# Kernel optimization log

Measured on AMD Instinct MI355X. Metric: run time of the kernel, lower is better.

The kernel has to match this reference:

```python
import jax, jax.numpy as jnp
import numpy as np

EPS = 1e-5
NH = 8          # num_heads
WT_LEVELS = 5


def ln(x, w, b):
    m = jnp.mean(x, -1, keepdims=True)
    v = jnp.mean((x - m) ** 2, -1, keepdims=True)
    return (x - m) / jnp.sqrt(v + EPS) * w + b


def gelu(x):
    return jax.nn.gelu(x, approximate=False)  # torch nn.GELU default (erf)


def dwconv(x, w, b, stride, padding):
    # x: [B,C,H,W], w: [kh,kw,1,C] depthwise
    C = x.shape[1]
    y = jax.lax.conv_general_dilated(x, w, (stride, stride), padding,
                                     dimension_numbers=('NCHW', 'HWIO', 'NCHW'),
                                     feature_group_count=C)
    return y if b is None else y + b[None, :, None, None]


def conv2d(x, w, b, padding='SAME'):
    y = jax.lax.conv_general_dilated(x, w, (1, 1), padding,
                                     dimension_numbers=('NCHW', 'HWIO', 'NCHW'))
    return y + b[None, :, None, None]


def haar_dwt(x):
    # orthonormal 2x2 Haar analysis via even/odd slicing (no conv needed)
    a = x[..., 0::2, 0::2]; b = x[..., 0::2, 1::2]
    c = x[..., 1::2, 0::2]; d = x[..., 1::2, 1::2]
    ll = (a + b + c + d) * 0.5
    lh = (-a - b + c + d) * 0.5
    hl = (-a + b - c + d) * 0.5
    hh = (a - b - c + d) * 0.5
    return ll, lh, hl, hh


def haar_idwt(ll, lh, hl, hh):
    a = (ll - lh - hl + hh) * 0.5
    b = (ll - lh + hl - hh) * 0.5
    c = (ll + lh - hl - hh) * 0.5
    d = (ll + lh + hl + hh) * 0.5
    B, C, H, W = ll.shape
    top = jnp.stack([a, b], -1).reshape(B, C, H, 2 * W)
    bot = jnp.stack([c, d], -1).reshape(B, C, H, 2 * W)
    return jnp.stack([top, bot], -2).reshape(B, C, 2 * H, 2 * W)


def wtconv(x, base_w, base_b, base_scale, wav_w, wav_scale):
    # WTConv2d (Haar, wt_levels=5, kernel 3, depthwise): multi-level wavelet
    # decomposition, depthwise 3x3 conv + scale at each level, reconstruction,
    # added to a scaled depthwise base conv.
    B, C = x.shape[0], x.shape[1]
    lls, hs, shapes = [], [], []
    cur = x
    for i in range(WT_LEVELS):
        shapes.append(cur.shape)
        Hc, Wc = cur.shape[2], cur.shape[3]
        if Hc % 2 or Wc % 2:
            cur = jnp.pad(cur, ((0, 0), (0, 0), (0, Hc % 2), (0, Wc % 2)))
        sub = jnp.stack(haar_dwt(cur), 2)                # [B,C,4,h,w]
        cur = sub[:, :, 0]
        h, w = sub.shape[3], sub.shape[4]
        t = sub.reshape(B, C * 4, h, w)
        t = dwconv(t, wav_w[i], None, 1, 'SAME') * wav_scale[i][None, :, None, None]
        t = t.reshape(B, C, 4, h, w)
        lls.append(t[:, :, 0])
        hs.append(t[:, :, 1:4])
    nxt = 0.0
    for i in range(WT_LEVELS - 1, -1, -1):
        ll = lls[i] + nxt
        h3 = hs[i]
        nxt = haar_idwt(ll, h3[:, :, 0], h3[:, :, 1], h3[:, :, 2])
        sh = shapes[i]
        nxt = nxt[:, :, :sh[2], :sh[3]]
    base = dwconv(x, base_w, base_b, 1, 'SAME') * base_scale[None, :, None, None]
    return base + nxt


def block_forward(x, H, W, ln1_w, ln1_b, ln2_w, ln2_b, q_w, kv1_w, kv2_w,
                  sr1_w, sr1_b, sr2_w, sr2_b, an1_w, an1_b, an2_w, an2_b,
                  wt_base_w, wt_base_b, wt_base_scale, wt_wav_w, wt_wav_scale,
                  cp2d_w, cp2d_b, cn_w, cn_b, proj_w, proj_b,
                  fc1_w, fc1_b, fc2_w, fc2_b):
    B, N, C0 = x.shape
    Cp = C0 // 4            # conv/wavelet part channels
    Ca = C0 - Cp            # attention part channels (3/4)
    hd = Ca // NH
    scale = hd ** -0.5

    xin = ln(x, ln1_w, ln1_b)
    xc, xa = xin[..., :Cp], xin[..., Cp:]

    # --- wavelet-conv branch ---
    xc = xc.reshape(B, H, W, Cp).transpose(0, 3, 1, 2)        # [B,Cp,H,W]
    xc = wtconv(xc, wt_base_w, wt_base_b, wt_base_scale, wt_wav_w, wt_wav_scale)
    xc = conv2d(xc, cp2d_w, cp2d_b, 'SAME')                   # k3 p1 (sr_ratio=8)
    xc = gelu(ln(xc.reshape(B, Cp, N).transpose(0, 2, 1), cn_w, cn_b))  # [B,N,Cp]

    # --- multi-scale spatial-reduction attention (sr_ratio=8) ---
    q = (xa @ q_w).reshape(B, N, NH, hd).transpose(0, 2, 1, 3)  # [B,NH,N,hd]
    x_ = xa.transpose(0, 2, 1).reshape(B, Ca, H, W)
    x1 = gelu(ln(dwconv(x_, sr1_w, sr1_b, 8, 'VALID').reshape(B, Ca, -1)
                 .transpose(0, 2, 1), an1_w, an1_b))           # [B,49,Ca]
    x2 = gelu(ln(dwconv(x_, sr2_w, sr2_b, 4, 'VALID').reshape(B, Ca, -1)
                 .transpose(0, 2, 1), an2_w, an2_b))           # [B,196,Ca]

    def branch(xs, kv_w, qh):
        L = xs.shape[1]
        kv = (xs @ kv_w).reshape(B, L, 2, NH // 2, hd).transpose(2, 0, 3, 1, 4)
        k, v = kv[0], kv[1]
        a = jax.nn.softmax(jnp.einsum('bhnd,bhld->bhnl', qh, k) * scale, axis=-1)
        return jnp.einsum('bhnl,bhld->bhnd', a, v).transpose(0, 2, 1, 3).reshape(B, N, Ca // 2)

    y1 = branch(x1, kv1_w, q[:, :NH // 2])
    y2 = branch(x2, kv2_w, q[:, NH // 2:])

    attn_out = jnp.concatenate([y1, y2, xc], -1) @ proj_w + proj_b

    x = x + attn_out
    m = ln(x, ln2_w, ln2_b)
    return x + (gelu(m @ fc1_w + fc1_b) @ fc2_w + fc2_b)


def setup_inputs() -> dict:
    key = jax.random.key(0)
    ks = jax.random.split(key, 16)
    B, H, W, C0 = 32, 56, 56, 128
    N = H * W
    Cp, Ca = C0 // 4, C0 // 4 * 3

    def nrm(k, shape, std=0.02):
        return jax.random.normal(k, shape, jnp.float32) * std

    return dict(
        x=jax.random.normal(ks[0], (B, N, C0), jnp.float32),
        H=H, W=W,
        ln1_w=jnp.ones((C0,)), ln1_b=jnp.zeros((C0,)),
        ln2_w=jnp.ones((C0,)), ln2_b=jnp.zeros((C0,)),
        q_w=nrm(ks[1], (Ca, Ca)),
        kv1_w=nrm(ks[2], (Ca, Ca)),
        kv2_w=nrm(ks[3], (Ca, Ca)),
        sr1_w=nrm(ks[4], (8, 8, 1, Ca), 0.05), sr1_b=jnp.zeros((Ca,)),
        sr2_w=nrm(ks[5], (4, 4, 1, Ca), 0.05), sr2_b=jnp.zeros((Ca,)),
        an1_w=jnp.ones((Ca,)), an1_b=jnp.zeros((Ca,)),
        an2_w=jnp.ones((Ca,)), an2_b=jnp.zeros((Ca,)),
        wt_base_w=nrm(ks[6], (3, 3, 1, Cp), 0.1), wt_base_b=jnp.zeros((Cp,)),
        wt_base_scale=jnp.ones((Cp,)),
        wt_wav_w=nrm(ks[7], (5, 3, 3, 1, 4 * Cp), 0.1),
        wt_wav_scale=jnp.full((5, 4 * Cp), 0.1, jnp.float32),
        cp2d_w=nrm(ks[8], (3, 3, Cp, Cp), 0.05), cp2d_b=jnp.zeros((Cp,)),
        cn_w=jnp.ones((Cp,)), cn_b=jnp.zeros((Cp,)),
        proj_w=nrm(ks[9], (C0, C0)), proj_b=jnp.zeros((C0,)),
        fc1_w=nrm(ks[10], (C0, 4 * C0)), fc1_b=jnp.zeros((4 * C0,)),
        fc2_w=nrm(ks[11], (4 * C0, C0)), fc2_b=jnp.zeros((C0,)),
    )


def reference(x, H, W, ln1_w, ln1_b, ln2_w, ln2_b, q_w, kv1_w, kv2_w,
              sr1_w, sr1_b, sr2_w, sr2_b, an1_w, an1_b, an2_w, an2_b,
              wt_base_w, wt_base_b, wt_base_scale, wt_wav_w, wt_wav_scale,
              cp2d_w, cp2d_b, cn_w, cn_b, proj_w, proj_b,
              fc1_w, fc1_b, fc2_w, fc2_b):
    return block_forward(x, H, W, ln1_w, ln1_b, ln2_w, ln2_b, q_w, kv1_w, kv2_w,
                         sr1_w, sr1_b, sr2_w, sr2_b, an1_w, an1_b, an2_w, an2_b,
                         wt_base_w, wt_base_b, wt_base_scale, wt_wav_w, wt_wav_scale,
                         cp2d_w, cp2d_b, cn_w, cn_b, proj_w, proj_b,
                         fc1_w, fc1_b, fc2_w, fc2_b)
```

## Files before the change

### kernel.cpp

```cpp
#include <hip/hip_runtime.h>
#include <hip/hip_bf16.h>
#include <math.h>

typedef __hip_bfloat16 bf16;
typedef __attribute__((ext_vector_type(8))) short bf16x8;
typedef __attribute__((ext_vector_type(4))) float f32x4;

#define Bc   32
#define Hc   56
#define Wcc  56
#define Nc   3136
#define Cpc  32
#define Cac  96
#define EPSc 1e-5f
#define SCALEc 0.28867513459481287f

__device__ __forceinline__ float gelu_f(float x) {
    return 0.5f * x * (1.0f + erff(x * 0.7071067811865475f));
}

__device__ __forceinline__ float fast_exp2(float x) {
#if defined(__has_builtin)
#if __has_builtin(__builtin_amdgcn_exp2f)
    return __builtin_amdgcn_exp2f(x);
#else
    return exp2f(x);
#endif
#else
    return exp2f(x);
#endif
}

__global__ __launch_bounds__(256) void ln1_kernel(const float* __restrict__ x,
        const float* __restrict__ g, const float* __restrict__ be,
        float* __restrict__ xa, bf16* __restrict__ xab, float* __restrict__ xc_img)
{
    int wv = threadIdx.x >> 6, lane = threadIdx.x & 63;
    int row = blockIdx.x * 4 + wv;
    if (row >= Bc * Nc) return;
    const float* xr = x + (size_t)row * 128;
    float x0 = xr[lane];
    float x1 = xr[lane + 64];
    float s = x0 + x1, q = x0 * x0 + x1 * x1;
    for (int o = 32; o; o >>= 1) { s += __shfl_xor(s, o); q += __shfl_xor(q, o); }
    float mean = s * (1.f / 128.f);
    float inv = rsqrtf(q * (1.f / 128.f) - mean * mean + EPSc);
    int b = row / Nc, n = row % Nc;
    {
        int c = lane;
        float y = (x0 - mean) * inv * g[c] + be[c];
        if (c < Cpc) xc_img[(size_t)(b * Cpc + c) * Nc + n] = y;
        else { xa[(size_t)row * Cac + (c - Cpc)] = y;
               xab[(size_t)row * Cac + (c - Cpc)] = __float2bfloat16(y); }
    }
    {
        int c = lane + 64;
        float y = (x1 - mean) * inv * g[c] + be[c];
        xa[(size_t)row * Cac + (c - Cpc)] = y;
        xab[(size_t)row * Cac + (c - Cpc)] = __float2bfloat16(y);
    }
}

__global__ void dwt_kernel(const float* __restrict__ src, int cs, int h, int w,
                           int h2, int w2, float* __restrict__ sub)
{
    int t = blockIdx.x * blockDim.x + threadIdx.x;
    int total = Bc * 32 * h2 * w2;
    if (t >= total) return;
    int xx = t % w2; int r = t / w2;
    int yy = r % h2; r /= h2;
    int c = r & 31; int b = r >> 5;
    const float* sp = src + (size_t)cs * (b * 32 + c) * h * w;
    int y0 = yy * 2, x0 = xx * 2;
    bool xe = (x0 + 1 < w), ye = (y0 + 1 < h);
    float a  = sp[y0 * w + x0];
    float bb = xe ? sp[y0 * w + x0 + 1] : 0.f;
    float cc = ye ? sp[(y0 + 1) * w + x0] : 0.f;
    float dd = (xe && ye) ? sp[(y0 + 1) * w + x0 + 1] : 0.f;
    size_t pl = (size_t)h2 * w2;
    size_t ob = (size_t)(b * 128 + c * 4) * pl + yy * w2 + xx;
    sub[ob]          = ( a + bb + cc + dd) * 0.5f;
    sub[ob + pl]     = (-a - bb + cc + dd) * 0.5f;
    sub[ob + 2 * pl] = (-a + bb - cc + dd) * 0.5f;
    sub[ob + 3 * pl] = ( a - bb - cc + dd) * 0.5f;
}

__global__ __launch_bounds__(256) void dwt234_kernel(const float* __restrict__ S1,
        float* __restrict__ S2, float* __restrict__ S3, float* __restrict__ S4)
{
    __shared__ float ll[196];
    int bc = blockIdx.x; int b = bc >> 5, c = bc & 31;
    int t = threadIdx.x;
    const float* src = S1 + (size_t)(b * 128 + c * 4) * 196;
    if (t < 196) ll[t] = src[t];
    __syncthreads();
    float l2 = 0.f;
    if (t < 49) {
        int yy = t / 7, xx = t % 7;
        int y0 = yy * 2, x0 = xx * 2;
        float a = ll[y0 * 14 + x0],       bb = ll[y0 * 14 + x0 + 1];
        float cc = ll[(y0 + 1) * 14 + x0], dd = ll[(y0 + 1) * 14 + x0 + 1];
        size_t ob = (size_t)(b * 128 + c * 4) * 49 + t;
        float vll = (a + bb + cc + dd) * 0.5f;
        S2[ob]       = vll;
        S2[ob + 49]  = (-a - bb + cc + dd) * 0.5f;
        S2[ob + 98]  = (-a + bb - cc + dd) * 0.5f;
        S2[ob + 147] = ( a - bb - cc + dd) * 0.5f;
        l2 = vll;
    }
    __syncthreads();
    if (t < 49) ll[t] = l2;
    __syncthreads();
    float l3 = 0.f;
    if (t < 16) {
        int yy = t >> 2, xx = t & 3;
        int y0 = yy * 2, x0 = xx * 2;
        bool xe = (x0 + 1 < 7), ye = (y0 + 1 < 7);
        float a  = ll[y0 * 7 + x0];
        float bb = xe ? ll[y0 * 7 + x0 + 1] : 0.f;
        float cc = ye ? ll[(y0 + 1) * 7 + x0] : 0.f;
        float dd = (xe && ye) ? ll[(y0 + 1) * 7 + x0 + 1] : 0.f;
        size_t ob = (size_t)(b * 128 + c * 4) * 16 + t;
        float vll = (a + bb + cc + dd) * 0.5f;
        S3[ob]      = vll;
        S3[ob + 16] = (-a - bb + cc + dd) * 0.5f;
        S3[ob + 32] = (-a + bb - cc + dd) * 0.5f;
        S3[ob + 48] = ( a - bb - cc + dd) * 0.5f;
        l3 = vll;
    }
    __syncthreads();
    if (t < 16) ll[t] = l3;
    __syncthreads();
    if (t < 4) {
        int yy = t >> 1, xx = t & 1;
        int y0 = yy * 2, x0 = xx * 2;
        float a = ll[y0 * 4 + x0],       bb = ll[y0 * 4 + x0 + 1];
        float cc = ll[(y0 + 1) * 4 + x0], dd = ll[(y0 + 1) * 4 + x0 + 1];
        size_t ob = (size_t)(b * 128 + c * 4) * 4 + t;
        S4[ob]      = ( a + bb + cc + dd) * 0.5f;
        S4[ob + 4]  = (-a - bb + cc + dd) * 0.5f;
        S4[ob + 8]  = (-a + bb - cc + dd) * 0.5f;
        S4[ob + 12] = ( a - bb - cc + dd) * 0.5f;
    }
}

template<int H>
__device__ __forceinline__ void dw3_body(int r, const float* __restrict__ src,
        const float* __restrict__ wt, const float* __restrict__ scale,
        float* __restrict__ dst)
{
    int x = r % H; int rr = r / H;
    int y = rr % H; rr /= H;
    int c = rr & 127;
    const float* sp = src + (r - x - y * H);
    float acc = 0.f;
    #pragma unroll
    for (int u = 0; u < 3; u++) {
        int yy = y + u - 1;
        if (yy < 0 || yy >= H) continue;
        #pragma unroll
        for (int v = 0; v < 3; v++) {
            int xx = x + v - 1;
            if (xx < 0 || xx >= H) continue;
            acc += sp[yy * H + xx] * wt[(u * 3 + v) * 128 + c];
        }
    }
    dst[r] = acc * scale[c];
}

__global__ void dw3x3_all_kernel(const float* __restrict__ sub, const float* __restrict__ wavw,
        const float* __restrict__ wavs, float* __restrict__ tt)
{
    int t = blockIdx.x * blockDim.x + threadIdx.x;
    if (t < 3211264)      dw3_body<28>(t,           sub,           wavw,        wavs,       tt);
    else if (t < 4014080) dw3_body<14>(t - 3211264, sub + 3211264, wavw + 1152, wavs + 128, tt + 3211264);
    else if (t < 4214784) dw3_body<7> (t - 4014080, sub + 4014080, wavw + 2304, wavs + 256, tt + 4014080);
    else if (t < 4280320) dw3_body<4> (t - 4214784, sub + 4214784, wavw + 3456, wavs + 384, tt + 4214784);
    else if (t < 4296704) dw3_body<2> (t - 4280320, sub + 4280320, wavw + 4608, wavs + 512, tt + 4280320);
}

__global__ __launch_bounds__(256) void idwt432_kernel(const float* __restrict__ T4,
        const float* __restrict__ T3, const float* __restrict__ T2,
        float* __restrict__ out14)
{
    __shared__ float rec[196];
    int bc = blockIdx.x; int b = bc >> 5, c = bc & 31;
    int t = threadIdx.x;
    float v4 = 0.f;
    if (t < 16) {
        int y = t >> 2, x = t & 3;
        int y2 = y >> 1, x2 = x >> 1;
        size_t base = (size_t)(b * 128 + c * 4) * 4 + y2 * 2 + x2;
        float ll = T4[base];
        float lh = T4[base + 4], hl = T4[base + 8], hh = T4[base + 12];
        float v;
        if ((y & 1) == 0) v = ((x & 1) == 0) ? (ll - lh - hl + hh) : (ll - lh + hl - hh);
        else              v = ((x & 1) == 0) ? (ll + lh - hl - hh) : (ll + lh + hl + hh);
        v4 = v * 0.5f;
    }
    if (t < 16) rec[t] = v4;
    __syncthreads();
    float v3 = 0.f;
    if (t < 49) {
        int y = t / 7, x = t % 7;
        int y2 = y >> 1, x2 = x >> 1;
        size_t base = (size_t)(b * 128 + c * 4) * 16 + y2 * 4 + x2;
        float ll = T3[base] + rec[y2 * 4 + x2];
        float lh = T3[base + 16], hl = T3[base + 32], hh = T3[base + 48];
        float v;
        if ((y & 1) == 0) v = ((x & 1) == 0) ? (ll - lh - hl + hh) : (ll - lh + hl - hh);
        else              v = ((x & 1) == 0) ? (ll + lh - hl - hh) : (ll + lh + hl + hh);
        v3 = v * 0.5f;
    }
    __syncthreads();
    if (t < 49) rec[t] = v3;
    __syncthreads();
    if (t < 196) {
        int y = t / 14, x = t % 14;
        int y2 = y >> 1, x2 = x >> 1;
        size_t base = (size_t)(b * 128 + c * 4) * 49 + y2 * 7 + x2;
        float ll = T2[base] + rec[y2 * 7 + x2];
        float lh = T2[base + 49], hl = T2[base + 98], hh = T2[base + 147];
        float v;
        if ((y & 1) == 0) v = ((x & 1) == 0) ? (ll - lh - hl + hh) : (ll - lh + hl - hh);
        else              v = ((x & 1) == 0) ? (ll + lh - hl - hh) : (ll + lh + hl + hh);
        out14[(size_t)(b * 32 + c) * 196 + t] = v * 0.5f;
    }
}

__global__ void idwt_kernel(const float* __restrict__ tl, const float* __restrict__ nxt,
        float* __restrict__ outp, int h2, int w2, int ho, int wo)
{
    int t = blockIdx.x * blockDim.x + threadIdx.x;
    int total = Bc * 32 * ho * wo;
    if (t >= total) return;
    int x = t % wo; int r = t / wo;
    int y = r % ho; r /= ho;
    int c = r & 31; int b = r >> 5;
    int y2 = y >> 1, x2 = x >> 1;
    size_t pl = (size_t)h2 * w2;
    size_t base = (size_t)(b * 128 + c * 4) * pl + y2 * w2 + x2;
    float ll = tl[base];
    if (nxt) ll += nxt[(size_t)(b * 32 + c) * pl + y2 * w2 + x2];
    float lh = tl[base + pl], hl = tl[base + 2 * pl], hh = tl[base + 3 * pl];
    float v;
    if ((y & 1) == 0) v = ((x & 1) == 0) ? (ll - lh - hl + hh) : (ll - lh + hl - hh);
    else              v = ((x & 1) == 0) ? (ll + lh - hl - hh) : (ll + lh + hl + hh);
    outp[t] = v * 0.5f;
}

__global__ void idwt_dwbase_kernel(const float* __restrict__ tl, const float* __restrict__ nxt,
        const float* __restrict__ src, const float* __restrict__ wt,
        const float* __restrict__ scale, const float* __restrict__ bias,
        bf16* __restrict__ dst_nhwc)
{
    int t = blockIdx.x * blockDim.x + threadIdx.x;
    if (t >= Bc * 32 * Nc) return;
    int x = t % Wcc; int r = t / Wcc;
    int y = r % Hc; r /= Hc;
    int c = r & 31; int b = r >> 5;
    int y2 = y >> 1, x2 = x >> 1;
    const size_t pl = 784;
    size_t base = (size_t)(b * 128 + c * 4) * pl + y2 * 28 + x2;
    float ll = tl[base] + nxt[(size_t)(b * 32 + c) * pl + y2 * 28 + x2];
    float lh = tl[base + pl], hl = tl[base + 2 * pl], hh = tl[base + 3 * pl];
    float v;
    if ((y & 1) == 0) v = ((x & 1) == 0) ? (ll - lh - hl + hh) : (ll - lh + hl - hh);
    else              v = ((x & 1) == 0) ? (ll + lh - hl - hh) : (ll + lh + hl + hh);
    float recon = v * 0.5f;
    const float* sp = src + (t - x - y * Wcc);
    float acc = 0.f;
    #pragma unroll
    for (int u = 0; u < 3; u++) {
        int yy = y + u - 1;
        if (yy < 0 || yy >= Hc) continue;
        #pragma unroll
        for (int vv2 = 0; vv2 < 3; vv2++) {
            int xx = x + vv2 - 1;
            if (xx < 0 || xx >= Wcc) continue;
            acc += sp[yy * Wcc + xx] * wt[(u * 3 + vv2) * 32 + c];
        }
    }
    acc = (acc + bias[c]) * scale[c] + recon;
    dst_nhwc[(((size_t)b * Hc + y) * Wcc + x) * 32 + c] = __float2bfloat16(acc);
}

__global__ void wprep_kernel(const float* __restrict__ qw, const float* __restrict__ kv1w,
        const float* __restrict__ kv2w, const float* __restrict__ pw,
        const float* __restrict__ f1w, const float* __restrict__ f2w,
        const float* __restrict__ cpw, bf16* __restrict__ qwt, bf16* __restrict__ kv1wt,
        bf16* __restrict__ kv2wt, bf16* __restrict__ pwt, bf16* __restrict__ w1t,
        bf16* __restrict__ w2t, bf16* __restrict__ cpwt)
{
    int t = blockIdx.x * blockDim.x + threadIdx.x;
    if (t < 9216) {
        int n = t % 96, k = t / 96;
        qwt[n * 96 + k] = __float2bfloat16(qw[t]);
    } else if (t < 18432) {
        int u = t - 9216; int n = u % 96, k = u / 96;
        kv1wt[n * 96 + k] = __float2bfloat16(kv1w[u]);
    } else if (t < 27648) {
        int u = t - 18432; int n = u % 96, k = u / 96;
        kv2wt[n * 96 + k] = __float2bfloat16(kv2w[u]);
    } else if (t < 44032) {
        int u = t - 27648; int n = u % 128, k = u / 128;
        pwt[n * 128 + k] = __float2bfloat16(pw[u]);
    } else if (t < 109568) {
        int u = t - 44032; int n = u % 512, k = u / 512;
        w1t[(size_t)n * 128 + k] = __float2bfloat16(f1w[u]);
    } else if (t < 175104) {
        int u = t - 109568; int n = u % 128, k = u / 128;
        w2t[(size_t)n * 512 + k] = __float2bfloat16(f2w[u]);
    } else if (t < 184320) {
        int u = t - 175104; int co = u / 288, k = u % 288;
        cpwt[u] = __float2bfloat16(cpw[k * 32 + co]);
    }
}

__global__ __launch_bounds__(256) void cp2d_cn_kernel(const bf16* __restrict__ src,
        const bf16* __restrict__ wtc, const float* __restrict__ bias,
        const float* __restrict__ cnw, const float* __restrict__ cnb,
        bf16* __restrict__ attn_cat)
{
    __shared__ unsigned short in_s[10 * 400];
    __shared__ unsigned short w_s[32 * 296];
    int tid = threadIdx.x;
    int b = blockIdx.y;
    int ty = blockIdx.x / 7, tx = blockIdx.x % 7;
    for (int idx = tid; idx < 1152; idx += 256) {
        int co = idx / 36, j8 = (idx % 36) * 8;
        *(int4*)&w_s[co * 296 + j8] = *(const int4*)(wtc + co * 288 + j8);
    }
    {
        int idx = tid;
        if (idx < 200) {
            int cell = idx >> 1, half = idx & 1;
            int dy = cell / 10, dx = cell % 10;
            int gy = ty * 8 - 1 + dy, gx = tx * 8 - 1 + dx;
            int4 v0 = make_int4(0, 0, 0, 0), v1 = v0;
            if (gy >= 0 && gy < 56 && gx >= 0 && gx < 56) {
                const int4* gp = (const int4*)(src + ((((size_t)b * 56 + gy) * 56 + gx) * 32 + half * 16));
                v0 = gp[0]; v1 = gp[1];
            }
            *(int4*)&in_s[dy * 400 + dx * 40 + half * 16] = v0;
            *(int4*)&in_s[dy * 400 + dx * 40 + half * 16 + 8] = v1;
        }
    }
    __syncthreads();
    int wave = tid >> 6, lane = tid & 63;
    int ml = lane & 15, qd = lane >> 4;
    int m = wave * 16 + ml;
    int ly = m >> 3, lx = m & 7;
    f32x4 acc0 = {0.f, 0.f, 0.f, 0.f}, acc1 = {0.f, 0.f, 0.f, 0.f};
    #pragma unroll
    for (int u = 0; u < 3; u++)
    #pragma unroll
    for (int v = 0; v < 3; v++) {
        bf16x8 af = *(const bf16x8*)&in_s[(ly + u) * 400 + (lx + v) * 40 + qd * 8];
        int k = (u * 3 + v) * 32 + qd * 8;
        bf16x8 b0 = *(const bf16x8*)&w_s[ml * 296 + k];
        bf16x8 b1 = *(const bf16x8*)&w_s[(16 + ml) * 296 + k];
        acc0 = __builtin_amdgcn_mfma_f32_16x16x32_bf16(af, b0, acc0, 0, 0, 0);
        acc1 = __builtin_amdgcn_mfma_f32_16x16x32_bf16(af, b1, acc1, 0, 0, 0);
    }
    float bia0 = bias[ml], bia1 = bias[16 + ml];
    float g0 = cnw[ml], g1 = cnw[16 + ml];
    float be0 = cnb[ml], be1 = cnb[16 + ml];
    #pragma unroll
    for (int r = 0; r < 4; r++) {
        float c0 = acc0[r] + bia0;
        float c1 = acc1[r] + bia1;
        float s = c0 + c1, q = c0 * c0 + c1 * c1;
        #pragma unroll
        for (int o = 8; o; o >>= 1) { s += __shfl_xor(s, o); q += __shfl_xor(q, o); }
        float mean = s * (1.f / 32.f);
        float inv = rsqrtf(q * (1.f / 32.f) - mean * mean + EPSc);
        int mr = wave * 16 + qd * 4 + r;
        int ry = ty * 8 + (mr >> 3), rx = tx * 8 + (mr & 7);
        bf16* op = attn_cat + ((size_t)b * Nc + ry * 56 + rx) * 128 + 96;
        op[ml]      = __float2bfloat16(gelu_f((c0 - mean) * inv * g0 + be0));
        op[16 + ml] = __float2bfloat16(gelu_f((c1 - mean) * inv * g1 + be1));
    }
}

template<int KS, int LD>
__device__ __forceinline__ void sr_body(int t, const float* __restrict__ xa,
        const float* __restrict__ wt, const float* __restrict__ bias,
        float* __restrict__ outp)
{
    int c = t % Cac; int r = t / Cac;
    int j = r % LD; r /= LD;
    int i = r % LD; int b = r / LD;
    float acc = bias[c];
    for (int u = 0; u < KS; u++)
        for (int v = 0; v < KS; v++)
            acc += xa[(size_t)(b * Nc + (i * KS + u) * Wcc + (j * KS + v)) * Cac + c]
                 * wt[(u * KS + v) * Cac + c];
    outp[t] = acc;
}

__global__ void sr_all_kernel(const float* __restrict__ xa,
        const float* __restrict__ sr1w, const float* __restrict__ sr1b, float* __restrict__ x1p,
        const float* __restrict__ sr2w, const float* __restrict__ sr2b, float* __restrict__ x2p)
{
    int t = blockIdx.x * blockDim.x + threadIdx.x;
    if (t < 150528) sr_body<8, 7>(t, xa, sr1w, sr1b, x1p);
    else {
        int u = t - 150528;
        if (u < 602112) sr_body<4, 14>(u, xa, sr2w, sr2b, x2p);
    }
}

__global__ __launch_bounds__(256) void ln96_all_kernel(
        const float* __restrict__ s1, const float* __restrict__ g1,
        const float* __restrict__ b1, bf16* __restrict__ d1,
        const float* __restrict__ s2, const float* __restrict__ g2,
        const float* __restrict__ b2, bf16* __restrict__ d2)
{
    int wv = threadIdx.x >> 6, lane = threadIdx.x & 63;
    int row = blockIdx.x * 4 + wv;
    const float* sp; const float* g; const float* be; bf16* dst; int r;
    if (row < 1568)      { sp = s1; g = g1; be = b1; dst = d1; r = row; }
    else if (row < 7840) { sp = s2; g = g2; be = b2; dst = d2; r = row - 1568; }
    else return;
    sp += (size_t)r * 96;
    float x0 = sp[lane];
    float x1 = (lane < 32) ? sp[64 + lane] : 0.f;
    float s = x0 + x1, q = x0 * x0 + x1 * x1;
    for (int o = 32; o; o >>= 1) { s += __shfl_xor(s, o); q += __shfl_xor(q, o); }
    float mean = s * (1.f / 96.f);
    float inv = rsqrtf(q * (1.f / 96.f) - mean * mean + EPSc);
    dst[(size_t)r * 96 + lane] =
        __float2bfloat16(gelu_f((x0 - mean) * inv * g[lane] + be[lane]));
    if (lane < 32)
        dst[(size_t)r * 96 + 64 + lane] =
            __float2bfloat16(gelu_f((x1 - mean) * inv * g[64 + lane] + be[64 + lane]));
}

template<int OMODE>
__device__ __forceinline__ void qkv_body(const bf16* __restrict__ A,
        const bf16* __restrict__ Wt, void* __restrict__ outp,
        int M, int m0, unsigned short (*As)[40], unsigned short (*Bs)[40], int tid)
{
    const int K = 96, Nt = 96;
    int wave = tid >> 6, lane = tid & 63;
    f32x4 acc[6];
    #pragma unroll
    for (int f = 0; f < 6; f++) acc[f] = (f32x4){0.f, 0.f, 0.f, 0.f};
    int ar = tid >> 2, ac = (tid & 3) << 3;
    int ml = wave * 16 + (lane & 15);
    int qd = lane >> 4;
    for (int k0 = 0; k0 < K; k0 += 32) {
        int4 av = make_int4(0, 0, 0, 0);
        if (m0 + ar < M) av = *(const int4*)(A + (size_t)(m0 + ar) * K + k0 + ac);
        *(int4*)&As[ar][ac] = av;
        for (int idx = tid; idx < 384; idx += 256) {
            int br = idx >> 2, bc = (idx & 3) << 3;
            *(int4*)&Bs[br][bc] = *(const int4*)(Wt + (size_t)br * K + k0 + bc);
        }
        __syncthreads();
        bf16x8 af = *(const bf16x8*)&As[ml][qd * 8];
        #pragma unroll
        for (int f = 0; f < 6; f++) {
            bf16x8 bfv = *(const bf16x8*)&Bs[f * 16 + (lane & 15)][qd * 8];
            acc[f] = __builtin_amdgcn_mfma_f32_16x16x32_bf16(af, bfv, acc[f], 0, 0, 0);
        }
        __syncthreads();
    }
    #pragma unroll
    for (int f = 0; f < 6; f++) {
        int n = f * 16 + (lane & 15);
        #pragma unroll
        for (int r = 0; r < 4; r++) {
            int m = m0 + wave * 16 + qd * 4 + r;
            if (m >= M) continue;
            float v = acc[f][r];
            if (OMODE == 2) {
                int b = m / Nc, nn = m - b * Nc;
                int h = n / 12, d = n - h * 12;
                ((float*)outp)[(((size_t)(b * 8 + h)) * Nc + nn) * 12 + d] = v;
            } else
                ((float*)outp)[(size_t)m * Nt + n] = v;
        }
    }
}

__global__ __launch_bounds__(256) void qkv_kernel(
        const bf16* __restrict__ XAb,  const bf16* __restrict__ qwt,   float* __restrict__ QB,
        const bf16* __restrict__ X1Bb, const bf16* __restrict__ kv1wt, float* __restrict__ KV1,
        const bf16* __restrict__ X2Bb, const bf16* __restrict__ kv2wt, float* __restrict__ KV2)
{
    __shared__ unsigned short As[64][40];
    __shared__ unsigned short Bs[96][40];
    int by = blockIdx.x;
    int tid = threadIdx.x;
    if (by < 1568)      qkv_body<2>(XAb,  qwt,   QB,  100352, by * 64,          As, Bs, tid);
    else if (by < 1593) qkv_body<0>(X1Bb, kv1wt, KV1, 1568,   (by - 1568) * 64, As, Bs, tid);
    else                qkv_body<0>(X2Bb, kv2wt, KV2, 6272,   (by - 1593) * 64, As, Bs, tid);
}

template<int NF, int BK, bool GELU, bool RES, int OMODE>
__global__ __launch_bounds__(256) void gemm_kernel(const bf16* __restrict__ A,
        const bf16* __restrict__ Wt, const float* __restrict__ bias,
        const float* __restrict__ res, void* __restrict__ outp,
        int M, int K, int Nt)
{
    constexpr int TN = 16 * NF;
    __shared__ unsigned short As[64][BK + 8];
    __shared__ unsigned short Bs[TN][BK + 8];
    int tid = threadIdx.x;
    int wave = tid >> 6, lane = tid & 63;
    int m0 = blockIdx.y * 64, n0 = blockIdx.x * TN;
    f32x4 acc[NF];
    #pragma unroll
    for (int f = 0; f < NF; f++) acc[f] = (f32x4){0.f, 0.f, 0.f, 0.f};

    int ar = tid >> 2, ac = (tid & 3) << 3;
    int ml = wave * 16 + (lane & 15);
    int qd = lane >> 4;

    for (int k0 = 0; k0 < K; k0 += BK) {
        #pragma unroll
        for (int i = 0; i < BK / 32; i++) {
            int cc = ac + i * 32;
            int4 av = make_int4(0, 0, 0, 0);
            if (m0 + ar < M) av = *(const int4*)(A + (size_t)(m0 + ar) * K + k0 + cc);
            *(int4*)&As[ar][cc] = av;
        }
        for (int idx = tid; idx < TN * (BK / 8); idx += 256) {
            int br = idx / (BK / 8), bc = (idx % (BK / 8)) * 8;
            *(int4*)&Bs[br][bc] = *(const int4*)(Wt + (size_t)(n0 + br) * K + k0 + bc);
        }
        __syncthreads();
        #pragma unroll
        for (int kk = 0; kk < BK / 32; kk++) {
            bf16x8 af = *(const bf16x8*)&As[ml][kk * 32 + qd * 8];
            #pragma unroll
            for (int f = 0; f < NF; f++) {
                bf16x8 bfv = *(const bf16x8*)&Bs[f * 16 + (lane & 15)][kk * 32 + qd * 8];
                acc[f] = __builtin_amdgcn_mfma_f32_16x16x32_bf16(af, bfv, acc[f], 0, 0, 0);
            }
        }
        __syncthreads();
    }
    #pragma unroll
    for (int f = 0; f < NF; f++) {
        int n = n0 + f * 16 + (lane & 15);
        #pragma unroll
        for (int r = 0; r < 4; r++) {
            int m = m0 + wave * 16 + qd * 4 + r;
            if (m >= M) continue;
            float v = acc[f][r];
            if (bias) v += bias[n];
            if (GELU) v = gelu_f(v);
            if (RES)  v += res[(size_t)m * Nt + n];
            if (OMODE == 1)
                ((bf16*)outp)[(size_t)m * Nt + n] = __float2bfloat16(v);
            else
                ((float*)outp)[(size_t)m * Nt + n] = v;
        }
    }
}

__global__ __launch_bounds__(256) void proj_ln_kernel(const bf16* __restrict__ A,
        const bf16* __restrict__ Wt, const float* __restrict__ bias,
        const float* __restrict__ res, const float* __restrict__ g,
        const float* __restrict__ be, float* __restrict__ xres, bf16* __restrict__ xnb)
{
    __shared__ unsigned short As[64][72];
    __shared__ unsigned short Bs[128][72];
    int tid = threadIdx.x;
    int wave = tid >> 6, lane = tid & 63;
    int m0 = blockIdx.x * 64;
    f32x4 acc[8];
    #pragma unroll
    for (int f = 0; f < 8; f++) acc[f] = (f32x4){0.f, 0.f, 0.f, 0.f};

    int ar = tid >> 2, ac = (tid & 3) << 3;
    int ml = lane & 15, qd = lane >> 4;
    int mlw = wave * 16 + ml;

    for (int k0 = 0; k0 < 128; k0 += 64) {
        #pragma unroll
        for (int i = 0; i < 2; i++) {
            int cc = ac + i * 32;
            *(int4*)&As[ar][cc] = *(const int4*)(A + (size_t)(m0 + ar) * 128 + k0 + cc);
        }
        for (int idx = tid; idx < 1024; idx += 256) {
            int br = idx >> 3, bc = (idx & 7) * 8;
            *(int4*)&Bs[br][bc] = *(const int4*)(Wt + (size_t)br * 128 + k0 + bc);
        }
        __syncthreads();
        #pragma unroll
        for (int kk = 0; kk < 2; kk++) {
            bf16x8 af = *(const bf16x8*)&As[mlw][kk * 32 + qd * 8];
            #pragma unroll
            for (int f = 0; f < 8; f++) {
                bf16x8 bfv = *(const bf16x8*)&Bs[f * 16 + ml][kk * 32 + qd * 8];
                acc[f] = __builtin_amdgcn_mfma_f32_16x16x32_bf16(af, bfv, acc[f], 0, 0, 0);
            }
        }
        __syncthreads();
    }
    float bia[8], gg[8], bb[8];
    #pragma unroll
    for (int f = 0; f < 8; f++) {
        int n = f * 16 + ml;
        bia[f] = bias[n]; gg[f] = g[n]; bb[f] = be[n];
    }
    #pragma unroll
    for (int r = 0; r < 4; r++) {
        int m = m0 + wave * 16 + qd * 4 + r;
        float vv[8];
        float s = 0.f, q = 0.f;
        #pragma unroll
        for (int f = 0; f < 8; f++) {
            int n = f * 16 + ml;
            float v = acc[f][r] + bia[f] + res[(size_t)m * 128 + n];
            vv[f] = v; s += v; q += v * v;
        }
        #pragma unroll
        for (int o = 8; o; o >>= 1) { s += __shfl_xor(s, o); q += __shfl_xor(q, o); }
        float mean = s * (1.f / 128.f);
        float inv = rsqrtf(q * (1.f / 128.f) - mean * mean + EPSc);
        #pragma unroll
        for (int f = 0; f < 8; f++) {
            int n = f * 16 + ml;
            xres[(size_t)m * 128 + n] = vv[f];
            xnb[(size_t)m * 128 + n] =
                __float2bfloat16((vv[f] - mean) * inv * gg[f] + bb[f]);
        }
    }
}

template<int L>
__device__ __forceinline__ void attn_body(const float* __restrict__ qh,
        const float* __restrict__ kv, int hl, int h, int b,
        float* kb, float* vb, bf16* __restrict__ attn_cat)
{
    for (int idx = threadIdx.x; idx < L * 3; idx += 256) {
        int l = idx / 3, f = idx % 3;
        const float4* kp = (const float4*)(kv + (size_t)(b * L + l) * 96 + hl * 12) + f;
        float4 kk = kp[0];
        float4 vv = kp[12];
        *(float4*)&kb[l * 12 + f * 4] = kk;
        *(float4*)&vb[l * 12 + f * 4] = vv;
    }
    int n = blockIdx.x * 256 + threadIdx.x;
    bool act = (n < Nc);
    int nn = act ? n : (Nc - 1);
    const float4* qp = (const float4*)(qh + (((size_t)(b * 8 + h)) * Nc + nn) * 12);
    float4 q0 = qp[0], q1 = qp[1], q2 = qp[2];
    const float PRE = SCALEc * 1.4426950408889634f;
    q0.x *= PRE; q0.y *= PRE; q0.z *= PRE; q0.w *= PRE;
    q1.x *= PRE; q1.y *= PRE; q1.z *= PRE; q1.w *= PRE;
    q2.x *= PRE; q2.y *= PRE; q2.z *= PRE; q2.w *= PRE;
    __syncthreads();

    float den = 0.f;
    float o[12];
    #pragma unroll
    for (int d = 0; d < 12; d++) o[d] = 0.f;

    #pragma unroll 4
    for (int l = 0; l < L; l++) {
        const float4 k0 = *(const float4*)&kb[l * 12];
        const float4 k1 = *(const float4*)&kb[l * 12 + 4];
        const float4 k2 = *(const float4*)&kb[l * 12 + 8];
        float s0 = q0.x * k0.x + q0.y * k0.y + q0.z * k0.z + q0.w * k0.w;
        float s1 = q1.x * k1.x + q1.y * k1.y + q1.z * k1.z + q1.w * k1.w;
        float s2 = q2.x * k2.x + q2.y * k2.y + q2.z * k2.z + q2.w * k2.w;
        float e = fast_exp2(s0 + s1 + s2);
        den += e;
        const float4 v0 = *(const float4*)&vb[l * 12];
        const float4 v1 = *(const float4*)&vb[l * 12 + 4];
        const float4 v2 = *(const float4*)&vb[l * 12 + 8];
        o[0] += e * v0.x; o[1]  += e * v0.y; o[2]  += e * v0.z; o[3]  += e * v0.w;
        o[4] += e * v1.x; o[5]  += e * v1.y; o[6]  += e * v1.z; o[7]  += e * v1.w;
        o[8] += e * v2.x; o[9]  += e * v2.y; o[10] += e * v2.z; o[11] += e * v2.w;
    }
    if (act) {
        float rden = 1.f / den;
        bf16* op = attn_cat + (size_t)(b * Nc + n) * 128 + h * 12;
        #pragma unroll
        for (int d = 0; d < 12; d++) op[d] = __float2bfloat16(o[d] * rden);
    }
}

__global__ __launch_bounds__(256) void attn_kernel(const float* __restrict__ qh,
        const float* __restrict__ kv1, const float* __restrict__ kv2,
        bf16* __restrict__ attn_cat)
{
    __shared__ float kb[196 * 12];
    __shared__ float vb[196 * 12];
    int h = blockIdx.y, b = blockIdx.z;
    if (h < 4) attn_body<49> (qh, kv1, h,     h, b, kb, vb, attn_cat);
    else       attn_body<196>(qh, kv2, h - 4, h, b, kb, vb, attn_cat);
}

extern "C" void kernel_launch(void* const* d_in, const int* in_sizes, int n_in,
                              void* d_out, int out_size, void* d_ws, size_t ws_size,
                              hipStream_t stream)
{
    const float* x    = (const float*)d_in[0];
    const float* ln1w = (const float*)d_in[3];
    const float* ln1b = (const float*)d_in[4];
    const float* ln2w = (const float*)d_in[5];
    const float* ln2b = (const float*)d_in[6];
    const float* qw   = (const float*)d_in[7];
    const float* kv1w = (const float*)d_in[8];
    const float* kv2w = (const float*)d_in[9];
    const float* sr1w = (const float*)d_in[10];
    const float* sr1b = (const float*)d_in[11];
    const float* sr2w = (const float*)d_in[12];
    const float* sr2b = (const float*)d_in[13];
    const float* an1w = (const float*)d_in[14];
    const float* an1b = (const float*)d_in[15];
    const float* an2w = (const float*)d_in[16];
    const float* an2b = (const float*)d_in[17];
    const float* wbw  = (const float*)d_in[18];
    const float* wbb  = (const float*)d_in[19];
    const float* wbs  = (const float*)d_in[20];
    const float* wavw = (const float*)d_in[21];
    const float* wavs = (const float*)d_in[22];
    const float* cpw  = (const float*)d_in[23];
    const float* cpb  = (const float*)d_in[24];
    const float* cnw  = (const float*)d_in[25];
    const float* cnb  = (const float*)d_in[26];
    const float* pw   = (const float*)d_in[27];
    const float* pb   = (const float*)d_in[28];
    const float* f1w  = (const float*)d_in[29];
    const float* f1b  = (const float*)d_in[30];
    const float* f2w  = (const float*)d_in[31];
    const float* f2b  = (const float*)d_in[32];
    float* dout = (float*)d_out;
    float* ws = (float*)d_ws;

    float* XA    = ws;
    float* QB    = ws + 9633792;
    float* XRES  = ws;
    bf16*  XNb   = (bf16*)(ws + 12845056);
    bf16*  XAb   = (bf16*)(ws + 19267584);
    bf16*  ACATb = (bf16*)(ws + 24084480);
    float* XCI   = ws + 30507008;
    float* SUB   = ws + 33718272;
    float* TT    = ws + 38014976;
    float* RA    = ws + 42311680;
    float* RB    = ws + 45522944;
    float* X1P   = ws + 48734208;
    float* X2P   = ws + 48884736;
    bf16*  X1Bb  = (bf16*)(ws + 49486848);
    bf16*  X2Bb  = (bf16*)(ws + 49562112);
    float* KV1   = ws + 49863168;
    float* KV2   = ws + 50013696;
    bf16*  WTB   = (bf16*)(ws + 50615808);
    bf16*  qwt   = WTB;
    bf16*  kv1wt = WTB + 9216;
    bf16*  kv2wt = WTB + 18432;
    bf16*  pwt   = WTB + 27648;
    bf16*  w1t   = WTB + 44032;
    bf16*  w2t   = WTB + 109568;
    bf16*  cpwt  = WTB + 175104;
    bf16*  Hb    = (bf16*)(ws + 24084480);
    bf16*  CIMGb = (bf16*)SUB;
    float* S0 = SUB;            float* T0 = TT;
    float* S1 = SUB + 3211264;  float* T1 = TT + 3211264;
    float* S2 = SUB + 4014080;  float* T2 = TT + 4014080;
    float* S3 = SUB + 4214784;  float* T3 = TT + 4214784;
    float* S4 = SUB + 4280320;  float* T4 = TT + 4280320;

    wprep_kernel<<<720, 256, 0, stream>>>(qw, kv1w, kv2w, pw, f1w, f2w, cpw,
                                          qwt, kv1wt, kv2wt, pwt, w1t, w2t, cpwt);

    ln1_kernel<<<25088, 256, 0, stream>>>(x, ln1w, ln1b, XA, XAb, XCI);

    dwt_kernel<<<3136, 256, 0, stream>>>(XCI, 1, 56, 56, 28, 28, S0);
    dwt_kernel<<<784,  256, 0, stream>>>(S0, 4, 28, 28, 14, 14, S1);
    dwt234_kernel<<<1024, 256, 0, stream>>>(S1, S2, S3, S4);

    dw3x3_all_kernel<<<16784, 256, 0, stream>>>(SUB, wavw, wavs, TT);

    idwt432_kernel<<<1024, 256, 0, stream>>>(T4, T3, T2, RA);
    idwt_kernel<<<3136, 256, 0, stream>>>(T1, RA, RB, 14, 14, 28, 28);

    idwt_dwbase_kernel<<<12544, 256, 0, stream>>>(T0, RB, XCI, wbw, wbs, wbb, CIMGb);

    cp2d_cn_kernel<<<dim3(49, 32), 256, 0, stream>>>(CIMGb, cpwt, cpb, cnw, cnb, ACATb);

    sr_all_kernel<<<2940, 256, 0, stream>>>(XA, sr1w, sr1b, X1P, sr2w, sr2b, X2P);

    ln96_all_kernel<<<1960, 256, 0, stream>>>(X1P, an1w, an1b, X1Bb,
                                              X2P, an2w, an2b, X2Bb);

    qkv_kernel<<<1691, 256, 0, stream>>>(XAb, qwt, QB, X1Bb, kv1wt, KV1, X2Bb, kv2wt, KV2);

    attn_kernel<<<dim3(13, 8, 32), 256, 0, stream>>>(QB, KV1, KV2, ACATb);

    proj_ln_kernel<<<1568, 256, 0, stream>>>(ACATb, pwt, pb, x, ln2w, ln2b, XRES, XNb);

    gemm_kernel<4,64,true,false,1><<<dim3(8, 1568), 256, 0, stream>>>(XNb, w1t, f1b, nullptr, Hb, 100352, 128, 512);

    gemm_kernel<4,64,false,true,0><<<dim3(2, 1568), 256, 0, stream>>>(Hb, w2t, f2b, XRES, dout, 100352, 512, 128);
}
```

Measured before the change: 592.4 us.

## Fuse wavelet decomposition and reconstruction levels into per-channel shared-memory kernels

Merges the three DWT launches into one kernel per (batch, channel) that keeps the LL band in shared memory across all five levels. It also merges the three IDWT launches plus the depthwise base conv into one kernel that stages the input plane and intermediate reconstructions in shared memory. This removes several launches and the global round trips for intermediate LL/reconstruction buffers. The trade-off is that parallelism drops to 1024 blocks with larger shared memory per block. The final NHWC bf16 store is strided by 32 channels, so its coalescing stays poor.

Result: faster. 570.1 us (-3.8%).

```diff
diff --git a/kernel.cpp b/kernel.cpp
--- a/kernel.cpp
+++ b/kernel.cpp
@@ -61,81 +61,81 @@
     }
 }
 
-__global__ void dwt_kernel(const float* __restrict__ src, int cs, int h, int w,
-                           int h2, int w2, float* __restrict__ sub)
-{
-    int t = blockIdx.x * blockDim.x + threadIdx.x;
-    int total = Bc * 32 * h2 * w2;
-    if (t >= total) return;
-    int xx = t % w2; int r = t / w2;
-    int yy = r % h2; r /= h2;
-    int c = r & 31; int b = r >> 5;
-    const float* sp = src + (size_t)cs * (b * 32 + c) * h * w;
-    int y0 = yy * 2, x0 = xx * 2;
-    bool xe = (x0 + 1 < w), ye = (y0 + 1 < h);
-    float a  = sp[y0 * w + x0];
-    float bb = xe ? sp[y0 * w + x0 + 1] : 0.f;
-    float cc = ye ? sp[(y0 + 1) * w + x0] : 0.f;
-    float dd = (xe && ye) ? sp[(y0 + 1) * w + x0 + 1] : 0.f;
-    size_t pl = (size_t)h2 * w2;
-    size_t ob = (size_t)(b * 128 + c * 4) * pl + yy * w2 + xx;
-    sub[ob]          = ( a + bb + cc + dd) * 0.5f;
-    sub[ob + pl]     = (-a - bb + cc + dd) * 0.5f;
-    sub[ob + 2 * pl] = (-a + bb - cc + dd) * 0.5f;
-    sub[ob + 3 * pl] = ( a - bb - cc + dd) * 0.5f;
-}
-
-__global__ __launch_bounds__(256) void dwt234_kernel(const float* __restrict__ S1,
-        float* __restrict__ S2, float* __restrict__ S3, float* __restrict__ S4)
-{
-    __shared__ float ll[196];
+__global__ __launch_bounds__(256) void dwt_all_kernel(const float* __restrict__ xci,
+        float* __restrict__ S0, float* __restrict__ S1, float* __restrict__ S2,
+        float* __restrict__ S3, float* __restrict__ S4)
+{
+    __shared__ float bufA[3136];
+    __shared__ float bufB[784];
     int bc = blockIdx.x; int b = bc >> 5, c = bc & 31;
     int t = threadIdx.x;
-    const float* src = S1 + (size_t)(b * 128 + c * 4) * 196;
-    if (t < 196) ll[t] = src[t];
-    __syncthreads();
-    float l2 = 0.f;
+    const float* src = xci + (size_t)(b * 32 + c) * 3136;
+    for (int i = t; i < 3136; i += 256) bufA[i] = src[i];
+    __syncthreads();
+    for (int p = t; p < 784; p += 256) {
+        int yy = p / 28, xx = p % 28;
+        int y0 = yy * 2, x0 = xx * 2;
+        float a = bufA[y0 * 56 + x0],        bb = bufA[y0 * 56 + x0 + 1];
+        float cc = bufA[(y0 + 1) * 56 + x0], dd = bufA[(y0 + 1) * 56 + x0 + 1];
+        size_t ob = (size_t)(b * 128 + c * 4) * 784 + p;
+        float vll = (a + bb + cc + dd) * 0.5f;
+        S0[ob]         = vll;
+        S0[ob + 784]   = (-a - bb + cc + dd) * 0.5f;
+        S0[ob + 1568]  = (-a + bb - cc + dd) * 0.5f;
+        S0[ob + 2352]  = ( a - bb - cc + dd) * 0.5f;
+        bufB[p] = vll;
+    }
+    __syncthreads();
+    for (int p = t; p < 196; p += 256) {
+        int yy = p / 14, xx = p % 14;
+        int y0 = yy * 2, x0 = xx * 2;
+        float a = bufB[y0 * 28 + x0],        bb = bufB[y0 * 28 + x0 + 1];
+        float cc = bufB[(y0 + 1) * 28 + x0], dd = bufB[(y0 + 1) * 28 + x0 + 1];
+        size_t ob = (size_t)(b * 128 + c * 4) * 196 + p;
+        float vll = (a + bb + cc + dd) * 0.5f;
+        S1[ob]       = vll;
+        S1[ob + 196] = (-a - bb + cc + dd) * 0.5f;
+        S1[ob + 392] = (-a + bb - cc + dd) * 0.5f;
+        S1[ob + 588] = ( a - bb - cc + dd) * 0.5f;
+        bufA[p] = vll;
+    }
+    __syncthreads();
     if (t < 49) {
         int yy = t / 7, xx = t % 7;
         int y0 = yy * 2, x0 = xx * 2;
-        float a = ll[y0 * 14 + x0],       bb = ll[y0 * 14 + x0 + 1];
-        float cc = ll[(y0 + 1) * 14 + x0], dd = ll[(y0 + 1) * 14 + x0 + 1];
+        float a = bufA[y0 * 14 + x0],        bb = bufA[y0 * 14 + x0 + 1];
+        float cc = bufA[(y0 + 1) * 14 + x0], dd = bufA[(y0 + 1) * 14 + x0 + 1];
         size_t ob = (size_t)(b * 128 + c * 4) * 49 + t;
         float vll = (a + bb + cc + dd) * 0.5f;
         S2[ob]       = vll;
         S2[ob + 49]  = (-a - bb + cc + dd) * 0.5f;
         S2[ob + 98]  = (-a + bb - cc + dd) * 0.5f;
         S2[ob + 147] = ( a - bb - cc + dd) * 0.5f;
-        l2 = vll;
-    }
-    __syncthreads();
-    if (t < 49) ll[t] = l2;
-    __syncthreads();
-    float l3 = 0.f;
+        bufB[t] = vll;
+    }
+    __syncthreads();
     if (t < 16) {
         int yy = t >> 2, xx = t & 3;
         int y0 = yy * 2, x0 = xx * 2;
         bool xe = (x0 + 1 < 7), ye = (y0 + 1 < 7);
-        float a  = ll[y0 * 7 + x0];
-        float bb = xe ? ll[y0 * 7 + x0 + 1] : 0.f;
-        float cc = ye ? ll[(y0 + 1) * 7 + x0] : 0.f;
-        float dd = (xe && ye) ? ll[(y0 + 1) * 7 + x0 + 1] : 0.f;
+        float a  = bufB[y0 * 7 + x0];
+        float bb = xe ? bufB[y0 * 7 + x0 + 1] : 0.f;
+        float cc = ye ? bufB[(y0 + 1) * 7 + x0] : 0.f;
+        float dd = (xe && ye) ? bufB[(y0 + 1) * 7 + x0 + 1] : 0.f;
         size_t ob = (size_t)(b * 128 + c * 4) * 16 + t;
         float vll = (a + bb + cc + dd) * 0.5f;
         S3[ob]      = vll;
         S3[ob + 16] = (-a - bb + cc + dd) * 0.5f;
         S3[ob + 32] = (-a + bb - cc + dd) * 0.5f;
         S3[ob + 48] = ( a - bb - cc + dd) * 0.5f;
-        l3 = vll;
-    }
-    __syncthreads();
-    if (t < 16) ll[t] = l3;
+        bufA[t] = vll;
+    }
     __syncthreads();
     if (t < 4) {
         int yy = t >> 1, xx = t & 1;
         int y0 = yy * 2, x0 = xx * 2;
-        float a = ll[y0 * 4 + x0],       bb = ll[y0 * 4 + x0 + 1];
-        float cc = ll[(y0 + 1) * 4 + x0], dd = ll[(y0 + 1) * 4 + x0 + 1];
+        float a = bufA[y0 * 4 + x0],        bb = bufA[y0 * 4 + x0 + 1];
+        float cc = bufA[(y0 + 1) * 4 + x0], dd = bufA[(y0 + 1) * 4 + x0 + 1];
         size_t ob = (size_t)(b * 128 + c * 4) * 4 + t;
         S4[ob]      = ( a + bb + cc + dd) * 0.5f;
         S4[ob + 4]  = (-a - bb + cc + dd) * 0.5f;
@@ -179,110 +179,96 @@
     else if (t < 4296704) dw3_body<2> (t - 4280320, sub + 4280320, wavw + 4608, wavs + 512, tt + 4280320);
 }
 
-__global__ __launch_bounds__(256) void idwt432_kernel(const float* __restrict__ T4,
-        const float* __restrict__ T3, const float* __restrict__ T2,
-        float* __restrict__ out14)
-{
-    __shared__ float rec[196];
+__global__ __launch_bounds__(256) void idwt_all_dwbase_kernel(
+        const float* __restrict__ T4, const float* __restrict__ T3,
+        const float* __restrict__ T2, const float* __restrict__ T1,
+        const float* __restrict__ T0, const float* __restrict__ xci,
+        const float* __restrict__ wt, const float* __restrict__ scale,
+        const float* __restrict__ bias, bf16* __restrict__ dst_nhwc)
+{
+    __shared__ float xs[3136];
+    __shared__ float r28[784];
+    __shared__ float rS[196];
     int bc = blockIdx.x; int b = bc >> 5, c = bc & 31;
     int t = threadIdx.x;
-    float v4 = 0.f;
+    const float* xsrc = xci + (size_t)(b * 32 + c) * 3136;
+    for (int i = t; i < 3136; i += 256) xs[i] = xsrc[i];
     if (t < 16) {
         int y = t >> 2, x = t & 3;
-        int y2 = y >> 1, x2 = x >> 1;
-        size_t base = (size_t)(b * 128 + c * 4) * 4 + y2 * 2 + x2;
+        size_t base = (size_t)(b * 128 + c * 4) * 4 + (y >> 1) * 2 + (x >> 1);
         float ll = T4[base];
         float lh = T4[base + 4], hl = T4[base + 8], hh = T4[base + 12];
         float v;
         if ((y & 1) == 0) v = ((x & 1) == 0) ? (ll - lh - hl + hh) : (ll - lh + hl - hh);
         else              v = ((x & 1) == 0) ? (ll + lh - hl - hh) : (ll + lh + hl + hh);
-        v4 = v * 0.5f;
-    }
-    if (t < 16) rec[t] = v4;
-    __syncthreads();
-    float v3 = 0.f;
+        rS[t] = v * 0.5f;
+    }
+    __syncthreads();
     if (t < 49) {
         int y = t / 7, x = t % 7;
         int y2 = y >> 1, x2 = x >> 1;
         size_t base = (size_t)(b * 128 + c * 4) * 16 + y2 * 4 + x2;
-        float ll = T3[base] + rec[y2 * 4 + x2];
+        float ll = T3[base] + rS[y2 * 4 + x2];
         float lh = T3[base + 16], hl = T3[base + 32], hh = T3[base + 48];
         float v;
         if ((y & 1) == 0) v = ((x & 1) == 0) ? (ll - lh - hl + hh) : (ll - lh + hl - hh);
         else              v = ((x & 1) == 0) ? (ll + lh - hl - hh) : (ll + lh + hl + hh);
-        v3 = v * 0.5f;
-    }
-    __syncthreads();
-    if (t < 49) rec[t] = v3;
+        r28[t] = v * 0.5f;
+    }
     __syncthreads();
     if (t < 196) {
         int y = t / 14, x = t % 14;
         int y2 = y >> 1, x2 = x >> 1;
         size_t base = (size_t)(b * 128 + c * 4) * 49 + y2 * 7 + x2;
-        float ll = T2[base] + rec[y2 * 7 + x2];
+        float ll = T2[base] + r28[y2 * 7 + x2];
         float lh = T2[base + 49], hl = T2[base + 98], hh = T2[base + 147];
         float v;
         if ((y & 1) == 0) v = ((x & 1) == 0) ? (ll - lh - hl + hh) : (ll - lh + hl - hh);
         else              v = ((x & 1) == 0) ? (ll + lh - hl - hh) : (ll + lh + hl + hh);
-        out14[(size_t)(b * 32 + c) * 196 + t] = v * 0.5f;
-    }
-}
-
-__global__ void idwt_kernel(const float* __restrict__ tl, const float* __restrict__ nxt,
-        float* __restrict__ outp, int h2, int w2, int ho, int wo)
-{
-    int t = blockIdx.x * blockDim.x + threadIdx.x;
-    int total = Bc * 32 * ho * wo;
-    if (t >= total) return;
-    int x = t % wo; int r = t / wo;
-    int y = r % ho; r /= ho;
-    int c = r & 31; int b = r >> 5;
-    int y2 = y >> 1, x2 = x >> 1;
-    size_t pl = (size_t)h2 * w2;
-    size_t base = (size_t)(b * 128 + c * 4) * pl + y2 * w2 + x2;
-    float ll = tl[base];
-    if (nxt) ll += nxt[(size_t)(b * 32 + c) * pl + y2 * w2 + x2];
-    float lh = tl[base + pl], hl = tl[base + 2 * pl], hh = tl[base + 3 * pl];
-    float v;
-    if ((y & 1) == 0) v = ((x & 1) == 0) ? (ll - lh - hl + hh) : (ll - lh + hl - hh);
-    else              v = ((x & 1) == 0) ? (ll + lh - hl - hh) : (ll + lh + hl + hh);
-    outp[t] = v * 0.5f;
-}
-
-__global__ void idwt_dwbase_kernel(const float* __restrict__ tl, const float* __restrict__ nxt,
-        const float* __restrict__ src, const float* __restrict__ wt,
-        const float* __restrict__ scale, const float* __restrict__ bias,
-        bf16* __restrict__ dst_nhwc)
-{
-    int t = blockIdx.x * blockDim.x + threadIdx.x;
-    if (t >= Bc * 32 * Nc) return;
-    int x = t % Wcc; int r = t / Wcc;
-    int y = r % Hc; r /= Hc;
-    int c = r & 31; int b = r >> 5;
-    int y2 = y >> 1, x2 = x >> 1;
-    const size_t pl = 784;
-    size_t base = (size_t)(b * 128 + c * 4) * pl + y2 * 28 + x2;
-    float ll = tl[base] + nxt[(size_t)(b * 32 + c) * pl + y2 * 28 + x2];
-    float lh = tl[base + pl], hl = tl[base + 2 * pl], hh = tl[base + 3 * pl];
-    float v;
-    if ((y & 1) == 0) v = ((x & 1) == 0) ? (ll - lh - hl + hh) : (ll - lh + hl - hh);
-    else              v = ((x & 1) == 0) ? (ll + lh - hl - hh) : (ll + lh + hl + hh);
-    float recon = v * 0.5f;
-    const float* sp = src + (t - x - y * Wcc);
-    float acc = 0.f;
-    #pragma unroll
-    for (int u = 0; u < 3; u++) {
-        int yy = y + u - 1;
-        if (yy < 0 || yy >= Hc) continue;
-        #pragma unroll
-        for (int vv2 = 0; vv2 < 3; vv2++) {
-            int xx = x + vv2 - 1;
-            if (xx < 0 || xx >= Wcc) continue;
-            acc += sp[yy * Wcc + xx] * wt[(u * 3 + vv2) * 32 + c];
-        }
-    }
-    acc = (acc + bias[c]) * scale[c] + recon;
-    dst_nhwc[(((size_t)b * Hc + y) * Wcc + x) * 32 + c] = __float2bfloat16(acc);
+        rS[t] = v * 0.5f;
+    }
+    __syncthreads();
+    for (int p = t; p < 784; p += 256) {
+        int y = p / 28, x = p % 28;
+        int y2 = y >> 1, x2 = x >> 1;
+        size_t base = (size_t)(b * 128 + c * 4) * 196 + y2 * 14 + x2;
+        float ll = T1[base] + rS[y2 * 14 + x2];
+        float lh = T1[base + 196], hl = T1[base + 392], hh = T1[base + 588];
+        float v;
+        if ((y & 1) == 0) v = ((x & 1) == 0) ? (ll - lh - hl + hh) : (ll - lh + hl - hh);
+        else              v = ((x & 1) == 0) ? (ll + lh - hl - hh) : (ll + lh + hl + hh);
+        r28[p] = v * 0.5f;
+    }
+    __syncthreads();
+    float w9[9];
+    #pragma unroll
+    for (int i = 0; i < 9; i++) w9[i] = wt[i * 32 + c];
+    float bia = bias[c], scl = scale[c];
+    for (int p = t; p < 3136; p += 256) {
+        int y = p / 56, x = p % 56;
+        int y2 = y >> 1, x2 = x >> 1;
+        size_t base = (size_t)(b * 128 + c * 4) * 784 + y2 * 28 + x2;
+        float ll = T0[base] + r28[y2 * 28 + x2];
+        float lh = T0[base + 784], hl = T0[base + 1568], hh = T0[base + 2352];
+        float v;
+        if ((y & 1) == 0) v = ((x & 1) == 0) ? (ll - lh - hl + hh) : (ll - lh + hl - hh);
+        else              v = ((x & 1) == 0) ? (ll + lh - hl - hh) : (ll + lh + hl + hh);
+        float recon = v * 0.5f;
+        float acc = 0.f;
+        #pragma unroll
+        for (int u = 0; u < 3; u++) {
+            int yy = y + u - 1;
+            if (yy < 0 || yy >= 56) continue;
+            #pragma unroll
+            for (int vv = 0; vv < 3; vv++) {
+                int xx = x + vv - 1;
+                if (xx < 0 || xx >= 56) continue;
+                acc += xs[yy * 56 + xx] * w9[u * 3 + vv];
+            }
+        }
+        acc = (acc + bia) * scl + recon;
+        dst_nhwc[(((size_t)b * 56 + y) * 56 + x) * 32 + c] = __float2bfloat16(acc);
+    }
 }
 
 __global__ void wprep_kernel(const float* __restrict__ qw, const float* __restrict__ kv1w,
@@ -745,8 +731,6 @@
     float* XCI   = ws + 30507008;
     float* SUB   = ws + 33718272;
     float* TT    = ws + 38014976;
-    float* RA    = ws + 42311680;
-    float* RB    = ws + 45522944;
     float* X1P   = ws + 48734208;
     float* X2P   = ws + 48884736;
     bf16*  X1Bb  = (bf16*)(ws + 49486848);
@@ -774,16 +758,12 @@
 
     ln1_kernel<<<25088, 256, 0, stream>>>(x, ln1w, ln1b, XA, XAb, XCI);
 
-    dwt_kernel<<<3136, 256, 0, stream>>>(XCI, 1, 56, 56, 28, 28, S0);
-    dwt_kernel<<<784,  256, 0, stream>>>(S0, 4, 28, 28, 14, 14, S1);
-    dwt234_kernel<<<1024, 256, 0, stream>>>(S1, S2, S3, S4);
+    dwt_all_kernel<<<1024, 256, 0, stream>>>(XCI, S0, S1, S2, S3, S4);
 
     dw3x3_all_kernel<<<16784, 256, 0, stream>>>(SUB, wavw, wavs, TT);
 
-    idwt432_kernel<<<1024, 256, 0, stream>>>(T4, T3, T2, RA);
-    idwt_kernel<<<3136, 256, 0, stream>>>(T1, RA, RB, 14, 14, 28, 28);
-
-    idwt_dwbase_kernel<<<12544, 256, 0, stream>>>(T0, RB, XCI, wbw, wbs, wbb, CIMGb);
+    idwt_all_dwbase_kernel<<<1024, 256, 0, stream>>>(T4, T3, T2, T1, T0, XCI,
+                                                     wbw, wbs, wbb, CIMGb);
 
     cp2d_cn_kernel<<<dim3(49, 32), 256, 0, stream>>>(CIMGb, cpwt, cpb, cnw, cnb, ACATb);
 
```
